# Optimization experiments

Hardware: AMD Instinct MI355X
Metric: run time of the kernel (lower is better)

Reference implementation:

```python
import jax, jax.numpy as jnp
import numpy as np

OBS, ACT, H, O, B = 256, 64, 1024, 8, 4096
ALPHA, GAMMA, ACT_LIMIT = 0.2, 0.99, 1.0
LOG_STD_MIN, LOG_STD_MAX = -20.0, 2.0
D = OBS + ACT + O  # intra-Q input dim


def setup_inputs() -> dict:
    key = jax.random.key(0)
    ks = iter(jax.random.split(key, 64))
    w = lambda shape: (jax.random.normal(next(ks), shape) * 0.05).astype(jnp.float32)
    inp = {}
    inp["state"] = jax.random.normal(next(ks), (B, OBS), jnp.float32)
    inp["action"] = jnp.tanh(jax.random.normal(next(ks), (B, ACT), jnp.float32))
    inp["next_state"] = jax.random.normal(next(ks), (B, OBS), jnp.float32)
    inp["reward"] = jax.random.normal(next(ks), (B, 1), jnp.float32)
    inp["done"] = jnp.zeros((B, 1), jnp.float32)
    inp["noise"] = jax.random.normal(next(ks), (B, ACT), jnp.float32)
    inp["option"] = jax.random.randint(next(ks), (B,), 0, O, jnp.int32)
    # online inter-Q (q1,q2 stacked on leading axis): obs -> H -> H -> O
    inp["interq_W1"], inp["interq_b1"] = w((2, OBS, H)), w((2, H))
    inp["interq_W2"], inp["interq_b2"] = w((2, H, H)), w((2, H))
    inp["interq_W3"], inp["interq_b3"] = w((2, H, O)), w((2, O))
    # target inter-Q
    inp["tinterq_W1"], inp["tinterq_b1"] = w((2, OBS, H)), w((2, H))
    inp["tinterq_W2"], inp["tinterq_b2"] = w((2, H, H)), w((2, H))
    inp["tinterq_W3"], inp["tinterq_b3"] = w((2, H, O)), w((2, O))
    # intra-Q (q1,q2 stacked): [obs,act,onehot] -> H -> H -> 1
    inp["intraq_W1"], inp["intraq_b1"] = w((2, D, H)), w((2, H))
    inp["intraq_W2"], inp["intraq_b2"] = w((2, H, H)), w((2, H))
    inp["intraq_W3"], inp["intraq_b3"] = w((2, H, 1)), w((2, 1))
    # per-option squashed-Gaussian policies: obs -> H -> H -> (mu, log_std)
    inp["pol_W1"], inp["pol_b1"] = w((O, OBS, H)), w((O, H))
    inp["pol_W2"], inp["pol_b2"] = w((O, H, H)), w((O, H))
    inp["pol_Wmu"], inp["pol_bmu"] = w((O, H, ACT)), w((O, ACT))
    inp["pol_Wls"], inp["pol_bls"] = w((O, H, ACT)), w((O, ACT))
    # per-option termination (beta) nets: obs -> H -> 1, sigmoid
    inp["beta_W1"], inp["beta_b1"] = w((O, OBS, H)), w((O, H))
    inp["beta_W2"], inp["beta_b2"] = w((O, H, 1)), w((O, 1))
    return inp


def _mlp2_k(x, W1, b1, W2, b2, W3, b3):
    # x: [B,in], params stacked over leading k -> [k,B,out]
    h = jax.nn.relu(jnp.einsum('bi,kih->kbh', x, W1) + b1[:, None, :])
    h = jax.nn.relu(jnp.einsum('kbh,khg->kbg', h, W2) + b2[:, None, :])
    return jnp.einsum('kbg,kgo->kbo', h, W3) + b3[:, None, :]


def _forward(state, action, next_state, reward, done, noise,
             interq_W1, interq_b1, interq_W2, interq_b2, interq_W3, interq_b3,
             tinterq_W1, tinterq_b1, tinterq_W2, tinterq_b2, tinterq_W3, tinterq_b3,
             intraq_W1, intraq_b1, intraq_W2, intraq_b2, intraq_W3, intraq_b3,
             pol_W1, pol_b1, pol_W2, pol_b2, pol_Wmu, pol_bmu, pol_Wls, pol_bls,
             beta_W1, beta_b1, beta_W2, beta_b2, option):
    idx = jnp.arange(state.shape[0])
    onehot = jax.nn.one_hot(option, O, dtype=state.dtype)
    # intra Q on (state, action, onehot)
    xq = jnp.concatenate([state, action, onehot], axis=-1)  # [B,D]
    q_intra = _mlp2_k(xq, intraq_W1, intraq_b1, intraq_W2, intraq_b2, intraq_W3, intraq_b3)
    q1_intra, q2_intra = q_intra[0], q_intra[1]  # [B,1]
    # option-routed policy: compute all options, gather top-1 (grouped-MoE form)
    h = jax.nn.relu(jnp.einsum('bi,oih->boh', state, pol_W1) + pol_b1)      # [B,O,H]
    h = jax.nn.relu(jnp.einsum('boh,ohg->bog', h, pol_W2) + pol_b2)         # [B,O,H]
    mu = (jnp.einsum('bog,oga->boa', h, pol_Wmu) + pol_bmu)[idx, option]    # [B,ACT]
    ls = (jnp.einsum('bog,oga->boa', h, pol_Wls) + pol_bls)[idx, option]
    ls = jnp.clip(ls, LOG_STD_MIN, LOG_STD_MAX)
    pre = mu + jnp.exp(ls) * noise  # reparameterized pre-tanh action
    LOG2PI = jnp.float32(np.log(2.0 * np.pi))
    logp = jnp.sum(-0.5 * noise**2 - ls - 0.5 * LOG2PI, axis=-1)
    logp = logp - jnp.sum(2.0 * (jnp.log(jnp.float32(2.0)) - pre - jax.nn.softplus(-2.0 * pre)), axis=-1)  # [B]
    current_actions = ACT_LIMIT * jnp.tanh(pre)  # [B,ACT]
    # option-routed termination prob on next_state
    hb = jax.nn.relu(jnp.einsum('bi,oih->boh', next_state, beta_W1) + beta_b1)
    blog = jnp.einsum('boh,oh->bo', hb, beta_W2[..., 0]) + beta_b2[:, 0]
    beta_prob = jax.nn.sigmoid(blog)[idx, option][:, None]  # [B,1]
    # TD target (no-grad in torch)
    q_t = _mlp2_k(next_state, tinterq_W1, tinterq_b1, tinterq_W2, tinterq_b2, tinterq_W3, tinterq_b3)
    q_inter_targ = jnp.minimum(q_t[0], q_t[1])  # [B,O]
    q_cur = q_inter_targ[idx, option][:, None]
    q_on = _mlp2_k(next_state, interq_W1, interq_b1, interq_W2, interq_b2, interq_W3, interq_b3)
    next_opt = jnp.argmax(jnp.minimum(q_on[0], q_on[1]), axis=-1)  # greedy next option
    q_next = q_inter_targ[idx, next_opt][:, None]
    bp = jax.lax.stop_gradient(beta_prob)
    backup = jax.lax.stop_gradient(
        reward + GAMMA * (1.0 - done) * ((1.0 - bp) * q_cur + bp * q_next))
    loss_intra_q = jnp.mean((q1_intra - backup) ** 2) + jnp.mean((q2_intra - backup) ** 2)
    q_pi = jax.lax.stop_gradient(jnp.minimum(q1_intra, q2_intra))[:, 0]
    loss_intra_pi = jnp.mean(ALPHA * logp - q_pi)
    return (loss_intra_q, loss_intra_pi, current_actions, logp, beta_prob)


def reference(state, action, next_state, reward, done, noise,
              interq_W1, interq_b1, interq_W2, interq_b2, interq_W3, interq_b3,
              tinterq_W1, tinterq_b1, tinterq_W2, tinterq_b2, tinterq_W3, tinterq_b3,
              intraq_W1, intraq_b1, intraq_W2, intraq_b2, intraq_W3, intraq_b3,
              pol_W1, pol_b1, pol_W2, pol_b2, pol_Wmu, pol_bmu, pol_Wls, pol_bls,
              beta_W1, beta_b1, beta_W2, beta_b2, option):
    return _forward(state, action, next_state, reward, done, noise,
                    interq_W1, interq_b1, interq_W2, interq_b2, interq_W3, interq_b3,
                    tinterq_W1, tinterq_b1, tinterq_W2, tinterq_b2, tinterq_W3, tinterq_b3,
                    intraq_W1, intraq_b1, intraq_W2, intraq_b2, intraq_W3, intraq_b3,
                    pol_W1, pol_b1, pol_W2, pol_b2, pol_Wmu, pol_bmu, pol_Wls, pol_bls,
                    beta_W1, beta_b1, beta_W2, beta_b2, option)
```

## Files before the change

### kernel.cpp

```cpp
#include <hip/hip_runtime.h>
#include <stdint.h>

#define B_SZ 4096
#define OBS 256
#define ACT 64
#define HID 1024
#define NOPT 8

typedef __attribute__((ext_vector_type(8))) short short8;
typedef __attribute__((ext_vector_type(4))) float floatx4;
typedef __attribute__((ext_vector_type(4))) unsigned int u32x4;

constexpr long long OFF_WT_I1 = 0;
constexpr long long OFF_WT_I2 = OFF_WT_I1 + 2LL*1024*256*2;
constexpr long long OFF_WT_T1 = OFF_WT_I2 + 2LL*1024*1024*2;
constexpr long long OFF_WT_T2 = OFF_WT_T1 + 2LL*1024*256*2;
constexpr long long OFF_WT_X1 = OFF_WT_T2 + 2LL*1024*1024*2;
constexpr long long OFF_WT_X2 = OFF_WT_X1 + 2LL*1024*384*2;
constexpr long long OFF_WT_P1 = OFF_WT_X2 + 2LL*1024*1024*2;
constexpr long long OFF_WT_P2 = OFF_WT_P1 + 8LL*1024*256*2;
constexpr long long OFF_WT_ML = OFF_WT_P2 + 8LL*1024*1024*2;
constexpr long long OFF_WT_B1 = OFF_WT_ML + 8LL*128*1024*2;
constexpr long long OFF_XQ    = OFF_WT_B1 + 8LL*1024*256*2;
constexpr long long OFF_NS    = OFF_XQ + 4096LL*384*2;
constexpr long long OFF_AGS   = OFF_NS + 4096LL*256*2;
constexpr long long OFF_AGN   = OFF_AGS + 4224LL*256*2;
constexpr long long OFF_HAX   = OFF_AGN + 4224LL*256*2;
constexpr long long OFF_HAI   = OFF_HAX + 2LL*4096*1024*2;
constexpr long long OFF_HAT   = OFF_HAI + 2LL*4096*1024*2;
constexpr long long OFF_HAP   = OFF_HAT + 2LL*4096*1024*2;
constexpr long long OFF_HAB   = OFF_HAP + 4224LL*1024*2;
constexpr long long OFF_HBP   = OFF_HAB + 4224LL*1024*2;
constexpr long long OFF_QI    = OFF_HBP + 4224LL*1024*2;
constexpr long long OFF_QON   = OFF_QI + 2LL*8*4096*4;
constexpr long long OFF_QT    = OFF_QON + 2LL*8*4096*8*4;
constexpr long long OFF_MULS  = OFF_QT + 2LL*8*4096*8*4;
constexpr long long OFF_PERM  = OFF_MULS + 4224LL*128*4;
constexpr long long OFF_OPTG  = OFF_PERM + 4096LL*4;
constexpr long long OFF_BP    = OFF_OPTG + ((4224LL*4 + 255) & ~255LL);
constexpr long long OFF_LOGP  = OFF_BP + 4096LL*4;
constexpr long long OFF_TILEB = OFF_LOGP + 4096LL*4;
constexpr long long OFF_TILEC = OFF_TILEB + 272LL*64;
constexpr long long OFF_TILED = OFF_TILEC + 232LL*64;
constexpr long long WS_TOTAL  = OFF_TILED + 40LL*64;

struct Tile {
  long long aOff, wOff, cOff;
  int mStart, mEnd, K, nCols, flags, biasSel, biasOff, redSel, redOff, pad0;
};
struct Ptrs { const float* bias[9]; const float* w3[3]; };
struct TrSrcs { const float* p[11]; };

__device__ __forceinline__ unsigned short f2bf(float x){
  union { float f; unsigned u; } v; v.f = x;
  unsigned r = v.u + 0x7fffu + ((v.u >> 16) & 1u);
  return (unsigned short)(r >> 16);
}
__device__ __forceinline__ float bf2f(unsigned short h){
  union { float f; unsigned u; } v; v.u = ((unsigned)h) << 16; return v.f;
}

__device__ const int tr_cum[12] = {0,512,2560,3072,5120,5888,7936,9984,18176,18688,19200,21248};
__device__ const int tr_gx[11]  = {8,32,8,32,12,32,8,32,32,32,8};
__device__ const int tr_K[11]   = {256,1024,256,1024,328,1024,256,1024,1024,1024,256};
__device__ const int tr_Kp[11]  = {256,1024,256,1024,384,1024,256,1024,1024,1024,256};
__device__ const int tr_N[11]   = {1024,1024,1024,1024,1024,1024,1024,1024,64,64,1024};
__device__ const long long tr_ws[11] = {256*1024,1024*1024,256*1024,1024*1024,328*1024,1024*1024,256*1024,1024*1024,1024*64,1024*64,256*1024};
__device__ const long long tr_ts[11] = {1024*256,1024*1024,1024*256,1024*1024,1024*384,1024*1024,1024*256,1024*1024,128*1024,128*1024,1024*256};
__device__ const long long tr_dst[11] = {OFF_WT_I1,OFF_WT_I2,OFF_WT_T1,OFF_WT_T2,OFF_WT_X1,OFF_WT_X2,OFF_WT_P1,OFF_WT_P2,OFF_WT_ML,OFF_WT_ML+64LL*1024*2,OFF_WT_B1};

__global__ void k_tr_all(char* __restrict__ wsB, TrSrcs srcs){
  int id = blockIdx.x, j = 0;
  while (id >= tr_cum[j+1]) j++;
  int tloc = id - tr_cum[j];
  int gx = tr_gx[j], gy = tr_N[j] >> 5;
  int per = gx*gy;
  int z = tloc / per, r = tloc % per;
  int kx = r % gx, ny = r / gx;
  int K = tr_K[j], Kpad = tr_Kp[j], N = tr_N[j];
  const float* src = srcs.p[j] + (long long)z * tr_ws[j];
  unsigned short* dst = (unsigned short*)(wsB + tr_dst[j]) + (long long)z * tr_ts[j];
  __shared__ float tile[32][33];
  int k0 = kx*32, n0 = ny*32;
  int tx = threadIdx.x, ty = threadIdx.y;
  #pragma unroll
  for (int i=0;i<4;i++){
    int k = k0 + ty + i*8;
    tile[ty+i*8][tx] = (k < K) ? src[(long long)k*N + n0 + tx] : 0.f;
  }
  __syncthreads();
  #pragma unroll
  for (int i=0;i<4;i++){
    int n = n0 + ty + i*8;
    dst[(long long)n*Kpad + k0 + tx] = f2bf(tile[tx][ty+i*8]);
  }
}

__global__ void k_route(char* __restrict__ wsB, const int* __restrict__ option,
                        float* __restrict__ out){
  __shared__ int cnt[NOPT], off[NOPT+1], cur[NOPT], ctiles[NOPT], toff[NOPT+1];
  int tid = threadIdx.x;
  int* perm = (int*)(wsB + OFF_PERM);
  int* optg = (int*)(wsB + OFF_OPTG);
  Tile* tb = (Tile*)(wsB + OFF_TILEB);
  Tile* tc = (Tile*)(wsB + OFF_TILEC);
  Tile* tdt = (Tile*)(wsB + OFF_TILED);
  if (tid < NOPT) cnt[tid] = 0;
  __syncthreads();
  for (int b = tid; b < B_SZ; b += 256) atomicAdd(&cnt[option[b]], 1);
  __syncthreads();
  if (tid == 0){
    off[0] = 0; toff[0] = 0;
    for (int o=0;o<NOPT;o++){
      off[o+1] = off[o] + cnt[o];
      ctiles[o] = (cnt[o] + 127) >> 7;
      toff[o+1] = toff[o] + ctiles[o];
      cur[o] = off[o];
    }
    out[0] = 0.f; out[1] = 0.f;
  }
  __syncthreads();
  for (int b = tid; b < B_SZ; b += 256){
    int o = option[b];
    int pos = atomicAdd(&cur[o], 1);
    perm[pos] = b; optg[pos] = o;
  }
  __syncthreads();
  if (tid < 192){
    int task = tid/32, mt = tid%32, z = task&1, net = task>>1;
    int ms = mt*128;
    Tile T{};
    T.mStart = ms; T.mEnd = 4096; T.nCols = 1024; T.flags = 0;
    T.redSel = 0; T.redOff = 0;
    if (net==0){ T.K=384; T.aOff = OFF_XQ + (long long)ms*768; T.wOff = OFF_WT_X1 + (long long)z*786432; T.cOff = OFF_HAX + (long long)z*8388608; T.biasSel=0; }
    else if (net==1){ T.K=256; T.aOff = OFF_NS + (long long)ms*512; T.wOff = OFF_WT_I1 + (long long)z*524288; T.cOff = OFF_HAI + (long long)z*8388608; T.biasSel=1; }
    else { T.K=256; T.aOff = OFF_NS + (long long)ms*512; T.wOff = OFF_WT_T1 + (long long)z*524288; T.cOff = OFF_HAT + (long long)z*8388608; T.biasSel=2; }
    T.biasOff = z*1024;
    tb[tid] = T;
    Tile C{};
    C.mStart = ms; C.mEnd = 4096; C.K = 1024; C.nCols = 1024;
    if (net==0){ C.flags=2; C.aOff = OFF_HAX + (long long)z*8388608 + (long long)ms*2048; C.wOff = OFF_WT_X2 + (long long)z*2097152; C.cOff = OFF_QI + (long long)z*131072; C.biasSel=5; C.redSel=0; C.redOff=z*1024; }
    else if (net==1){ C.flags=3; C.aOff = OFF_HAI + (long long)z*8388608 + (long long)ms*2048; C.wOff = OFF_WT_I2 + (long long)z*2097152; C.cOff = OFF_QON + (long long)z*1048576; C.biasSel=6; C.redSel=1; C.redOff=z*8192; }
    else { C.flags=3; C.aOff = OFF_HAT + (long long)z*8388608 + (long long)ms*2048; C.wOff = OFF_WT_T2 + (long long)z*2097152; C.cOff = OFF_QT + (long long)z*1048576; C.biasSel=7; C.redSel=2; C.redOff=z*8192; }
    C.biasOff = z*1024;
    tc[tid] = C;
  }
  if (tid < NOPT){
    int o = tid, base = toff[o], gs = off[o], ge = off[o+1];
    for (int t=0; t<ctiles[o]; t++){
      int ms = gs + t*128;
      Tile P{};
      P.mStart=ms; P.mEnd=ge; P.K=256; P.nCols=1024; P.flags=0;
      P.aOff = OFF_AGS + (long long)ms*512; P.wOff = OFF_WT_P1 + (long long)o*524288;
      P.cOff = OFF_HAP; P.biasSel=3; P.biasOff=o*1024;
      tb[192 + base + t] = P;
      Tile Bt{};
      Bt.mStart=ms; Bt.mEnd=ge; Bt.K=256; Bt.nCols=1024; Bt.flags=0;
      Bt.aOff = OFF_AGN + (long long)ms*512; Bt.wOff = OFF_WT_B1 + (long long)o*524288;
      Bt.cOff = OFF_HAB; Bt.biasSel=4; Bt.biasOff=o*1024;
      tb[232 + base + t] = Bt;
      Tile C2{};
      C2.mStart=ms; C2.mEnd=ge; C2.K=1024; C2.nCols=1024; C2.flags=0;
      C2.aOff = OFF_HAP + (long long)ms*2048; C2.wOff = OFF_WT_P2 + (long long)o*2097152;
      C2.cOff = OFF_HBP; C2.biasSel=8; C2.biasOff=o*1024;
      tc[192 + base + t] = C2;
      Tile M{};
      M.mStart=ms; M.mEnd=ge; M.K=1024; M.nCols=128; M.flags=1;
      M.aOff = OFF_HBP + (long long)ms*2048; M.wOff = OFF_WT_ML + (long long)o*262144;
      M.cOff = OFF_MULS; M.biasSel=-1;
      tdt[base + t] = M;
    }
  }
  __syncthreads();
  int tT = toff[NOPT];
  for (int s = tT + tid; s < 40; s += 256){
    tb[192+s].K = 0; tb[232+s].K = 0; tc[192+s].K = 0; tdt[s].K = 0;
  }
}

__global__ void k_prep(char* __restrict__ wsB, const float* __restrict__ state,
                       const float* __restrict__ action, const float* __restrict__ nstate,
                       const int* __restrict__ option){
  int blk = blockIdx.x, tid = threadIdx.x;
  const int* perm = (const int*)(wsB + OFF_PERM);
  if (blk < 4224){
    unsigned short* agS = (unsigned short*)(wsB + OFF_AGS);
    unsigned short* agN = (unsigned short*)(wsB + OFF_AGN);
    long long o = (long long)blk*256 + tid;
    if (blk < 4096){
      long long src = (long long)perm[blk]*256 + tid;
      agS[o] = f2bf(state[src]); agN[o] = f2bf(nstate[src]);
    } else { agS[o] = 0; agN[o] = 0; }
  } else if (blk < 8320){
    int b = blk - 4224;
    unsigned short* xq = (unsigned short*)(wsB + OFF_XQ);
    for (int c = tid; c < 384; c += 256){
      float v;
      if (c < 256) v = state[(long long)b*256 + c];
      else if (c < 320) v = action[(long long)b*64 + (c-256)];
      else if (c < 328) v = (option[b] == (c-320)) ? 1.f : 0.f;
      else v = 0.f;
      xq[(long long)b*384 + c] = f2bf(v);
    }
  } else {
    long long i = (long long)(blk-8320)*1024 + tid;
    unsigned short* nsb = (unsigned short*)(wsB + OFF_NS);
    #pragma unroll
    for (int k=0;k<4;k++){ nsb[i] = f2bf(nstate[i]); i += 256; }
  }
}

__global__ __launch_bounds__(256, 2)
void k_gemm(char* __restrict__ wsB, long long tileOff, Ptrs ptrs){
  __shared__ unsigned short As[128*64];
  __shared__ unsigned short Bs[256*64];
  Tile t = ((const Tile*)(wsB + tileOff))[blockIdx.y];
  if (t.K == 0) return;
  int n0 = blockIdx.x * 256;
  if (n0 >= t.nCols) return;

  int tid = threadIdx.x;
  int wave = tid >> 6, lane = tid & 63;
  int wm = wave & 1, wn = wave >> 1;
  int quad = lane >> 4, l16 = lane & 15;

  const floatx4 fzero = {0.f,0.f,0.f,0.f};
  floatx4 acc[4][8];
  #pragma unroll
  for (int mi=0;mi<4;mi++)
    #pragma unroll
    for (int ni=0;ni<8;ni++) acc[mi][ni] = fzero;

  long long rowBytes = (long long)t.K*2;
  const char* Abase = wsB + t.aOff;
  const char* Bbase = wsB + t.wOff + (long long)n0*rowBytes;

  int ra0 = tid >> 2, ka0 = (tid & 3) * 16;
  int ra1 = ra0 + 64;
  const char* gA0 = Abase + (long long)ra0*rowBytes + ka0;
  const char* gA1 = Abase + (long long)ra1*rowBytes + ka0;
  const char* gBp[4];
  #pragma unroll
  for (int j=0;j<4;j++){
    int rb = (tid >> 2) + j*64;
    gBp[j] = Bbase + (long long)rb*rowBytes + ka0;
  }

  u32x4 pA[4], pB[8];
  #define PREFETCH(KBB) { \
    long long _kb = (KBB); \
    pA[0] = *(const u32x4*)(gA0 + _kb);      pA[1] = *(const u32x4*)(gA0 + _kb + 64); \
    pA[2] = *(const u32x4*)(gA1 + _kb);      pA[3] = *(const u32x4*)(gA1 + _kb + 64); \
    _Pragma("unroll") \
    for (int j=0;j<4;j++){ \
      pB[2*j]   = *(const u32x4*)(gBp[j] + _kb); \
      pB[2*j+1] = *(const u32x4*)(gBp[j] + _kb + 64); \
    } }
  #define STAGE() { \
    *(u32x4*)((char*)As + tid*16)         = pA[0]; \
    *(u32x4*)((char*)As + 8192 + tid*16)  = pA[1]; \
    *(u32x4*)((char*)As + 4096 + tid*16)  = pA[2]; \
    *(u32x4*)((char*)As + 12288 + tid*16) = pA[3]; \
    _Pragma("unroll") \
    for (int j=0;j<4;j++){ \
      *(u32x4*)((char*)Bs + j*4096 + tid*16)         = pB[2*j]; \
      *(u32x4*)((char*)Bs + 16384 + j*4096 + tid*16) = pB[2*j+1]; \
    } }

  int nkb = t.K >> 6;
  PREFETCH(0);
  STAGE();
  __syncthreads();
  for (int kb = 0; kb < nkb; kb++){
    if (kb + 1 < nkb) PREFETCH((long long)(kb+1)*128);
    #pragma unroll
    for (int h=0; h<2; h++){
      short8 af[4], bfr[8];
      #pragma unroll
      for (int mi=0;mi<4;mi++)
        af[mi] = *(const short8*)((const char*)As + h*8192 + (wm*64 + mi*16 + l16)*64 + quad*16);
      #pragma unroll
      for (int ni=0;ni<8;ni++)
        bfr[ni] = *(const short8*)((const char*)Bs + h*16384 + (wn*128 + ni*16 + l16)*64 + quad*16);
      #pragma unroll
      for (int mi=0;mi<4;mi++)
        #pragma unroll
        for (int ni=0;ni<8;ni++)
          acc[mi][ni] = __builtin_amdgcn_mfma_f32_16x16x32_bf16(af[mi], bfr[ni], acc[mi][ni], 0, 0, 0);
    }
    __syncthreads();
    if (kb + 1 < nkb){
      STAGE();
      __syncthreads();
    }
  }
  #undef PREFETCH
  #undef STAGE

  if (t.flags <= 1){
    const float* bz = (t.biasSel >= 0) ? (ptrs.bias[t.biasSel] + t.biasOff) : nullptr;
    #pragma unroll
    for (int ni=0;ni<8;ni++){
      int col = n0 + wn*128 + ni*16 + l16;
      if (col >= t.nCols) continue;
      float bval = bz ? bz[col] : 0.f;
      #pragma unroll
      for (int mi=0;mi<4;mi++){
        int rbase = t.mStart + wm*64 + mi*16 + quad*4;
        floatx4 v = acc[mi][ni];
        #pragma unroll
        for (int r=0;r<4;r++){
          int grow = rbase + r;
          if (grow < t.mEnd){
            float x = v[r] + bval;
            if (t.flags == 0){
              x = fmaxf(x, 0.f);
              ((unsigned short*)(wsB + t.cOff))[(long long)grow*t.nCols + col] = f2bf(x);
            } else {
              ((float*)(wsB + t.cOff))[(long long)grow*t.nCols + col] = x;
            }
          }
        }
      }
    }
  } else {
    int NC = (t.flags == 2) ? 1 : 8;
    const float* w3 = ptrs.w3[t.redSel] + t.redOff;
    const float* bz = ptrs.bias[t.biasSel] + t.biasOff;
    int sl = blockIdx.x*2 + wn;
    float* red = (float*)(wsB + t.cOff) + (long long)sl*4096*NC;
    float bv[8]; int colv[8];
    #pragma unroll
    for (int ni=0;ni<8;ni++){ colv[ni] = n0 + wn*128 + ni*16 + l16; bv[ni] = bz[colv[ni]]; }
    #pragma unroll
    for (int mi=0;mi<4;mi++){
      #pragma unroll
      for (int r=0;r<4;r++){
        int row = t.mStart + wm*64 + mi*16 + quad*4 + r;
        float v[8];
        #pragma unroll
        for (int c=0;c<8;c++) v[c] = 0.f;
        #pragma unroll
        for (int ni=0;ni<8;ni++){
          float x = fmaxf(acc[mi][ni][r] + bv[ni], 0.f);
          if (NC == 1) v[0] += x * w3[colv[ni]];
          else {
            #pragma unroll
            for (int c=0;c<8;c++) v[c] += x * w3[colv[ni]*8 + c];
          }
        }
        for (int c=0;c<NC;c++){
          float s = v[c];
          s += __shfl_xor(s,1); s += __shfl_xor(s,2); s += __shfl_xor(s,4); s += __shfl_xor(s,8);
          if (l16 == 0 && row < t.mEnd) red[(long long)row*NC + c] = s;
        }
      }
    }
  }
}

__global__ void k_bp(char* __restrict__ wsB, const float* __restrict__ noise,
                     const float* __restrict__ bmu, const float* __restrict__ bls,
                     const float* __restrict__ beW2, const float* __restrict__ beb2,
                     float* __restrict__ out){
  int job = blockIdx.x*4 + (threadIdx.x >> 6);
  int lane = threadIdx.x & 63;
  const int* perm = (const int*)(wsB + OFF_PERM);
  const int* optg = (const int*)(wsB + OFF_OPTG);
  if (job < B_SZ){
    int i = job, o = optg[i], b = perm[i];
    const float* muls = (const float*)(wsB + OFF_MULS);
    float* logp = (float*)(wsB + OFF_LOGP);
    float mu = muls[(long long)i*128 + lane] + bmu[o*ACT + lane];
    float ls = muls[(long long)i*128 + 64 + lane] + bls[o*ACT + lane];
    ls = fminf(fmaxf(ls, -20.f), 2.f);
    float nv = noise[(long long)b*ACT + lane];
    float pre = mu + expf(ls)*nv;
    out[2 + (long long)b*ACT + lane] = tanhf(pre);
    float xx = -2.f*pre;
    float sp = fmaxf(xx, 0.f) + log1pf(expf(-fabsf(xx)));
    const float LOG2PI = 1.8378770664093453f;
    const float LN2 = 0.6931471805599453f;
    float lp = -0.5f*nv*nv - ls - 0.5f*LOG2PI - 2.f*(LN2 - pre - sp);
    for (int s=32;s;s>>=1) lp += __shfl_xor(lp, s);
    if (lane == 0){ out[2 + (long long)B_SZ*ACT + b] = lp; logp[b] = lp; }
  } else {
    int i = job - B_SZ, o = optg[i], b = perm[i];
    const char* hrow = wsB + OFF_HAB + (long long)i*2048;
    const float* w = beW2 + (long long)o*HID;
    float* bp = (float*)(wsB + OFF_BP);
    short8 v0 = *(const short8*)(hrow + lane*16);
    short8 v1 = *(const short8*)(hrow + 1024 + lane*16);
    float acc = 0.f;
    #pragma unroll
    for (int e=0;e<8;e++){
      acc += bf2f((unsigned short)v0[e]) * w[lane*8 + e];
      acc += bf2f((unsigned short)v1[e]) * w[512 + lane*8 + e];
    }
    for (int s=32;s;s>>=1) acc += __shfl_xor(acc, s);
    if (lane == 0){
      float v = 1.f/(1.f + expf(-(acc + beb2[o])));
      out[2 + (long long)B_SZ*ACT + B_SZ + b] = v; bp[b] = v;
    }
  }
}

__global__ void k_td(const char* __restrict__ wsB, const int* __restrict__ option,
                     const float* __restrict__ reward, const float* __restrict__ done,
                     const float* __restrict__ xb3, const float* __restrict__ ib3,
                     const float* __restrict__ tb3, float* __restrict__ out){
  int b = blockIdx.x*256 + threadIdx.x;
  const float* qiP  = (const float*)(wsB + OFF_QI);
  const float* qonP = (const float*)(wsB + OFF_QON);
  const float* qtP  = (const float*)(wsB + OFF_QT);
  const float* bp   = (const float*)(wsB + OFF_BP);
  const float* logp = (const float*)(wsB + OFF_LOGP);
  float q1 = xb3[0], q2 = xb3[1];
  #pragma unroll
  for (int sl=0; sl<8; sl++){
    q1 += qiP[sl*4096 + b];
    q2 += qiP[32768 + sl*4096 + b];
  }
  float qons[2][8], qts[2][8];
  #pragma unroll
  for (int z=0;z<2;z++)
    #pragma unroll
    for (int o=0;o<8;o++){ qons[z][o] = ib3[z*8+o]; qts[z][o] = tb3[z*8+o]; }
  for (int z=0;z<2;z++){
    for (int sl=0; sl<8; sl++){
      long long base = ((long long)(z*8 + sl)*4096 + b)*8;
      #pragma unroll
      for (int o=0;o<8;o++){ qons[z][o] += qonP[base+o]; qts[z][o] += qtP[base+o]; }
    }
  }
  float qitv[NOPT];
  #pragma unroll
  for (int o=0;o<NOPT;o++) qitv[o] = fminf(qts[0][o], qts[1][o]);
  float qcur = qitv[option[b]];
  float best = -1e30f; int bo = 0;
  #pragma unroll
  for (int o=0;o<NOPT;o++){
    float v = fminf(qons[0][o], qons[1][o]);
    if (v > best){ best = v; bo = o; }
  }
  float qnext = qitv[bo];
  float bpv = bp[b];
  float backup = reward[b] + 0.99f*(1.f - done[b])*((1.f - bpv)*qcur + bpv*qnext);
  float d1 = q1 - backup, d2 = q2 - backup;
  float tq = d1*d1 + d2*d2;
  float qpi = fminf(q1, q2);
  float tp = 0.2f*logp[b] - qpi;
  for (int s=32;s;s>>=1){ tq += __shfl_xor(tq, s); tp += __shfl_xor(tp, s); }
  __shared__ float sq[4], sp2[4];
  int wave = threadIdx.x>>6, lane = threadIdx.x&63;
  if (lane==0){ sq[wave]=tq; sp2[wave]=tp; }
  __syncthreads();
  if (threadIdx.x==0){
    atomicAdd(&out[0], (sq[0]+sq[1]+sq[2]+sq[3])/(float)B_SZ);
    atomicAdd(&out[1], (sp2[0]+sp2[1]+sp2[2]+sp2[3])/(float)B_SZ);
  }
}

extern "C" void kernel_launch(void* const* d_in, const int* in_sizes, int n_in,
                              void* d_out, int out_size, void* d_ws, size_t ws_size,
                              hipStream_t stream){
  const float* state  = (const float*)d_in[0];
  const float* action = (const float*)d_in[1];
  const float* nstate = (const float*)d_in[2];
  const float* reward = (const float*)d_in[3];
  const float* done   = (const float*)d_in[4];
  const float* noise  = (const float*)d_in[5];
  const int*   option = (const int*)d_in[6];
  const float* iq_W1 = (const float*)d_in[7];  const float* iq_b1 = (const float*)d_in[8];
  const float* iq_W2 = (const float*)d_in[9];  const float* iq_b2 = (const float*)d_in[10];
  const float* iq_W3 = (const float*)d_in[11]; const float* iq_b3 = (const float*)d_in[12];
  const float* tq_W1 = (const float*)d_in[13]; const float* tq_b1 = (const float*)d_in[14];
  const float* tq_W2 = (const float*)d_in[15]; const float* tq_b2 = (const float*)d_in[16];
  const float* tq_W3 = (const float*)d_in[17]; const float* tq_b3 = (const float*)d_in[18];
  const float* xw_W1 = (const float*)d_in[19]; const float* xw_b1 = (const float*)d_in[20];
  const float* xw_W2 = (const float*)d_in[21]; const float* xw_b2 = (const float*)d_in[22];
  const float* xw_W3 = (const float*)d_in[23]; const float* xw_b3 = (const float*)d_in[24];
  const float* p_W1 = (const float*)d_in[25];  const float* p_b1 = (const float*)d_in[26];
  const float* p_W2 = (const float*)d_in[27];  const float* p_b2 = (const float*)d_in[28];
  const float* p_Wmu = (const float*)d_in[29]; const float* p_bmu = (const float*)d_in[30];
  const float* p_Wls = (const float*)d_in[31]; const float* p_bls = (const float*)d_in[32];
  const float* be_W1 = (const float*)d_in[33]; const float* be_b1 = (const float*)d_in[34];
  const float* be_W2 = (const float*)d_in[35]; const float* be_b2 = (const float*)d_in[36];
  float* out = (float*)d_out;
  char* wsB = (char*)d_ws;
  if ((long long)ws_size < WS_TOTAL) return;

  TrSrcs trs;
  trs.p[0]=iq_W1; trs.p[1]=iq_W2; trs.p[2]=tq_W1; trs.p[3]=tq_W2; trs.p[4]=xw_W1;
  trs.p[5]=xw_W2; trs.p[6]=p_W1; trs.p[7]=p_W2; trs.p[8]=p_Wmu; trs.p[9]=p_Wls; trs.p[10]=be_W1;
  Ptrs ptrs;
  ptrs.bias[0]=xw_b1; ptrs.bias[1]=iq_b1; ptrs.bias[2]=tq_b1; ptrs.bias[3]=p_b1; ptrs.bias[4]=be_b1;
  ptrs.bias[5]=xw_b2; ptrs.bias[6]=iq_b2; ptrs.bias[7]=tq_b2; ptrs.bias[8]=p_b2;
  ptrs.w3[0]=xw_W3; ptrs.w3[1]=iq_W3; ptrs.w3[2]=tq_W3;

  k_route<<<1, 256, 0, stream>>>(wsB, option, out);
  k_tr_all<<<21248, dim3(32,8), 0, stream>>>(wsB, trs);
  k_prep<<<9344, 256, 0, stream>>>(wsB, state, action, nstate, option);
  k_gemm<<<dim3(4,272), 256, 0, stream>>>(wsB, OFF_TILEB, ptrs);
  k_gemm<<<dim3(4,232), 256, 0, stream>>>(wsB, OFF_TILEC, ptrs);
  k_gemm<<<dim3(1,40), 256, 0, stream>>>(wsB, OFF_TILED, ptrs);
  k_bp<<<2048, 256, 0, stream>>>(wsB, noise, p_bmu, p_bls, be_W2, be_b2, out);
  k_td<<<B_SZ/256, 256, 0, stream>>>(wsB, option, reward, done, xw_b3, iq_b3, tq_b3, out);
}
```

Before: 501.5 us.

## Widen weight transpose tiles and remap GEMM blocks across XCDs

The fp32-to-bf16 weight transpose kernel now uses 64x64 tiles with float4 loads and 32-byte packed bf16 stores, and launches four times fewer blocks. The aim is to cut the per-block overhead and the narrow 2-byte stores of the old 32x32 transpose. The GEMM kernel also remaps its linear block id so that neighbouring tile rows land on the same XCD when the tile count is a multiple of 8. That should improve L2 reuse of the shared A/B operands. The remap adds some index arithmetic, and the transpose's LDS reads in the second phase may cause bank conflicts.

```diff
diff --git a/kernel.cpp b/kernel.cpp
--- a/kernel.cpp
+++ b/kernel.cpp
@@ -60,40 +60,51 @@
   union { float f; unsigned u; } v; v.u = ((unsigned)h) << 16; return v.f;
 }
 
-__device__ const int tr_cum[12] = {0,512,2560,3072,5120,5888,7936,9984,18176,18688,19200,21248};
-__device__ const int tr_gx[11]  = {8,32,8,32,12,32,8,32,32,32,8};
-__device__ const int tr_K[11]   = {256,1024,256,1024,328,1024,256,1024,1024,1024,256};
-__device__ const int tr_Kp[11]  = {256,1024,256,1024,384,1024,256,1024,1024,1024,256};
-__device__ const int tr_N[11]   = {1024,1024,1024,1024,1024,1024,1024,1024,64,64,1024};
 __device__ const long long tr_ws[11] = {256*1024,1024*1024,256*1024,1024*1024,328*1024,1024*1024,256*1024,1024*1024,1024*64,1024*64,256*1024};
 __device__ const long long tr_ts[11] = {1024*256,1024*1024,1024*256,1024*1024,1024*384,1024*1024,1024*256,1024*1024,128*1024,128*1024,1024*256};
 __device__ const long long tr_dst[11] = {OFF_WT_I1,OFF_WT_I2,OFF_WT_T1,OFF_WT_T2,OFF_WT_X1,OFF_WT_X2,OFF_WT_P1,OFF_WT_P2,OFF_WT_ML,OFF_WT_ML+64LL*1024*2,OFF_WT_B1};
 
-__global__ void k_tr_all(char* __restrict__ wsB, TrSrcs srcs){
+__device__ const int t2_cum[12] = {0,128,640,768,1280,1472,1984,2496,4544,4672,4800,5312};
+__device__ const int t2_nk[11]  = {4,16,4,16,6,16,4,16,16,16,4};
+__device__ const int t2_N[11]   = {1024,1024,1024,1024,1024,1024,1024,1024,64,64,1024};
+__device__ const int t2_K[11]   = {256,1024,256,1024,328,1024,256,1024,1024,1024,256};
+__device__ const int t2_Kp[11]  = {256,1024,256,1024,384,1024,256,1024,1024,1024,256};
+
+__global__ __launch_bounds__(256)
+void k_tr(char* __restrict__ wsB, TrSrcs srcs){
+  __shared__ float lds[64*68];
   int id = blockIdx.x, j = 0;
-  while (id >= tr_cum[j+1]) j++;
-  int tloc = id - tr_cum[j];
-  int gx = tr_gx[j], gy = tr_N[j] >> 5;
-  int per = gx*gy;
-  int z = tloc / per, r = tloc % per;
-  int kx = r % gx, ny = r / gx;
-  int K = tr_K[j], Kpad = tr_Kp[j], N = tr_N[j];
+  while (id >= t2_cum[j+1]) j++;
+  int t = id - t2_cum[j];
+  int nk = t2_nk[j], nn = t2_N[j] >> 6;
+  int per = nk*nn;
+  int z = t / per, r = t % per;
+  int kt = r % nk, nt = r / nk;
+  int K = t2_K[j], Kp = t2_Kp[j], N = t2_N[j];
   const float* src = srcs.p[j] + (long long)z * tr_ws[j];
   unsigned short* dst = (unsigned short*)(wsB + tr_dst[j]) + (long long)z * tr_ts[j];
-  __shared__ float tile[32][33];
-  int k0 = kx*32, n0 = ny*32;
-  int tx = threadIdx.x, ty = threadIdx.y;
+  int k0 = kt*64, n0 = nt*64;
+  int tid = threadIdx.x;
+  int kl = tid >> 2, nc = tid & 3;
+  int krow = k0 + kl;
+  const float* s = src + (long long)krow*N + n0 + nc*16;
   #pragma unroll
   for (int i=0;i<4;i++){
-    int k = k0 + ty + i*8;
-    tile[ty+i*8][tx] = (k < K) ? src[(long long)k*N + n0 + tx] : 0.f;
-  }
-  __syncthreads();
-  #pragma unroll
-  for (int i=0;i<4;i++){
-    int n = n0 + ty + i*8;
-    dst[(long long)n*Kpad + k0 + tx] = f2bf(tile[tx][ty+i*8]);
-  }
+    float4 v = (krow < K) ? *(const float4*)(s + i*4) : make_float4(0.f,0.f,0.f,0.f);
+    *(float4*)(&lds[kl*68 + nc*16 + i*4]) = v;
+  }
+  __syncthreads();
+  int nl = tid >> 2, kc = tid & 3;
+  unsigned int w[8];
+  #pragma unroll
+  for (int p=0;p<8;p++){
+    float a = lds[(kc*16 + 2*p)*68 + nl];
+    float b = lds[(kc*16 + 2*p + 1)*68 + nl];
+    w[p] = (unsigned)f2bf(a) | ((unsigned)f2bf(b) << 16);
+  }
+  u32x4 o0 = {w[0],w[1],w[2],w[3]}, o1 = {w[4],w[5],w[6],w[7]};
+  char* d = (char*)(dst + (long long)(n0+nl)*Kp + k0 + kc*16);
+  *(u32x4*)d = o0; *(u32x4*)(d + 16) = o1;
 }
 
 __global__ void k_route(char* __restrict__ wsB, const int* __restrict__ option,
@@ -214,9 +225,16 @@
 void k_gemm(char* __restrict__ wsB, long long tileOff, Ptrs ptrs){
   __shared__ unsigned short As[128*64];
   __shared__ unsigned short Bs[256*64];
-  Tile t = ((const Tile*)(wsB + tileOff))[blockIdx.y];
+  int nx = gridDim.x, T = gridDim.y;
+  int id = blockIdx.y*nx + blockIdx.x;
+  int xb, yt;
+  if ((T & 7) == 0){
+    int xcd = id & 7, g = id >> 3;
+    xb = g % nx; yt = (g / nx) * 8 + xcd;
+  } else { xb = blockIdx.x; yt = blockIdx.y; }
+  Tile t = ((const Tile*)(wsB + tileOff))[yt];
   if (t.K == 0) return;
-  int n0 = blockIdx.x * 256;
+  int n0 = xb * 256;
   if (n0 >= t.nCols) return;
 
   int tid = threadIdx.x;
@@ -327,7 +345,7 @@
     int NC = (t.flags == 2) ? 1 : 8;
     const float* w3 = ptrs.w3[t.redSel] + t.redOff;
     const float* bz = ptrs.bias[t.biasSel] + t.biasOff;
-    int sl = blockIdx.x*2 + wn;
+    int sl = xb*2 + wn;
     float* red = (float*)(wsB + t.cOff) + (long long)sl*4096*NC;
     float bv[8]; int colv[8];
     #pragma unroll
@@ -499,7 +517,7 @@
   ptrs.w3[0]=xw_W3; ptrs.w3[1]=iq_W3; ptrs.w3[2]=tq_W3;
 
   k_route<<<1, 256, 0, stream>>>(wsB, option, out);
-  k_tr_all<<<21248, dim3(32,8), 0, stream>>>(wsB, trs);
+  k_tr<<<5312, 256, 0, stream>>>(wsB, trs);
   k_prep<<<9344, 256, 0, stream>>>(wsB, state, action, nstate, option);
   k_gemm<<<dim3(4,272), 256, 0, stream>>>(wsB, OFF_TILEB, ptrs);
   k_gemm<<<dim3(4,232), 256, 0, stream>>>(wsB, OFF_TILEC, ptrs);
```

Result: faster. 485.2 us (-3.2%).
